# Optimization experiments

Measured on AMD Instinct MI355X. Metric: run time of the kernel, lower is better.

The kernel has to match this reference:

```python
import jax, jax.numpy as jnp
import numpy as np

B, S, V, H = 32, 512, 32, 128
EPS = 1e-5

def _ln(h, w, b):
    m = jnp.mean(h, axis=-1, keepdims=True)
    var = jnp.mean((h - m) ** 2, axis=-1, keepdims=True)
    return (h - m) * jax.lax.rsqrt(var + EPS) * w + b

def setup_inputs() -> dict:
    key = jax.random.key(0)
    ks = jax.random.split(key, 24)
    n = lambda k, shp: jax.random.normal(k, shp, dtype=jnp.float32) * 0.05
    return {
        "x": jax.random.normal(ks[0], (B, S, V), dtype=jnp.float32),
        # flattened GRN (input_dim=V -> H)
        "fw1": n(ks[1], (H, V)), "fb1": jnp.zeros((H,), jnp.float32),
        "fw2": n(ks[2], (H, H)), "fb2": jnp.zeros((H,), jnp.float32),
        "fgw": n(ks[3], (H, H)), "fgb": jnp.zeros((H,), jnp.float32),
        "fsw": n(ks[4], (H, V)), "fsb": jnp.zeros((H,), jnp.float32),
        "flnw": jnp.ones((H,), jnp.float32), "flnb": jnp.zeros((H,), jnp.float32),
        # V per-variable GRNs (input_dim=1 -> H), stacked on leading V axis
        "vw1": n(ks[5], (V, H)), "vb1": jnp.zeros((V, H), jnp.float32),
        "vw2": n(ks[6], (V, H, H)), "vb2": jnp.zeros((V, H), jnp.float32),
        "vgw": n(ks[7], (V, H, H)), "vgb": jnp.zeros((V, H), jnp.float32),
        "vsw": n(ks[8], (V, H)), "vsb": jnp.zeros((V, H), jnp.float32),
        "vlnw": jnp.ones((V, H), jnp.float32), "vlnb": jnp.zeros((V, H), jnp.float32),
    }

def reference(x, fw1, fb1, fw2, fb2, fgw, fgb, fsw, fsb, flnw, flnb,
              vw1, vb1, vw2, vb2, vgw, vgb, vsw, vsb, vlnw, vlnb):
    # ---- flattened GRN -> variable weights ----
    h = jax.nn.elu(jnp.einsum('bsv,hv->bsh', x, fw1) + fb1)
    h = jnp.einsum('bsh,kh->bsk', h, fw2) + fb2
    g = jax.nn.sigmoid(jnp.einsum('bsh,kh->bsk', h, fgw) + fgb)
    skip = jnp.einsum('bsv,hv->bsh', x, fsw) + fsb
    w_out = _ln(g * h + (1.0 - g) * skip, flnw, flnb)        # [B,S,H]
    weights = jax.nn.softmax(w_out[..., :V], axis=-1)        # [B,S,V]
    # ---- per-variable GRNs, batched over V ----
    xe = x[..., None]                                         # [B,S,V,1]
    hv = jax.nn.elu(xe * vw1 + vb1)                           # [B,S,V,H]
    hv = jnp.einsum('bsvh,vkh->bsvk', hv, vw2) + vb2
    gv = jax.nn.sigmoid(jnp.einsum('bsvh,vkh->bsvk', hv, vgw) + vgb)
    skipv = xe * vsw + vsb                                    # [B,S,V,H]
    vout = _ln(gv * hv + (1.0 - gv) * skipv, vlnw, vlnb)      # [B,S,V,H]
    # ---- softmax-weighted combination ----
    selected = jnp.einsum('bsvh,bsv->bsh', vout, weights)     # [B,S,H]
    return selected, weights
```

## Files before the change

### kernel.cpp

```cpp
#include <hip/hip_runtime.h>
#include <hip/hip_bf16.h>

typedef __bf16 bf16_t;
typedef __bf16 bf16x8 __attribute__((ext_vector_type(8)));
typedef float  f32x4  __attribute__((ext_vector_type(4)));

#define DEVFN static __device__ __forceinline__

constexpr int TOK   = 32 * 512;
constexpr int W_OFF = TOK * 128;

constexpr size_t WS_A_VW2 = 0;
constexpr size_t WS_A_WG2 = (size_t)1 << 20;
constexpr size_t WS_BG2   = (size_t)2 << 20;
constexpr size_t WS_A_FW2 = ((size_t)2 << 20) + (64u  << 10);
constexpr size_t WS_A_WG1 = ((size_t)2 << 20) + (128u << 10);
constexpr size_t WS_BG1   = ((size_t)2 << 20) + (192u << 10);
constexpr size_t WS_A_FW1 = ((size_t)2 << 20) + (224u << 10);
constexpr size_t WS_A_FSW = ((size_t)2 << 20) + (256u << 10);
constexpr size_t WS_PART  = (size_t)3 << 20;
constexpr size_t PART_SZ  = (size_t)TOK * 128 * 4;

DEVFN float eluf(float z)  { return z > 0.0f ? z : (__expf(z) - 1.0f); }
DEVFN float sigmf(float z) { return __builtin_amdgcn_rcpf(1.0f + __expf(-z)); }
DEVFN unsigned short f2bfu(float f){ bf16_t h = (bf16_t)f; return __builtin_bit_cast(unsigned short, h); }

DEVFN uint4 pack8(f32x4 a, f32x4 b){
  uint4 r;
  r.x = (unsigned)f2bfu(a[0]) | ((unsigned)f2bfu(a[1]) << 16);
  r.y = (unsigned)f2bfu(a[2]) | ((unsigned)f2bfu(a[3]) << 16);
  r.z = (unsigned)f2bfu(b[0]) | ((unsigned)f2bfu(b[1]) << 16);
  r.w = (unsigned)f2bfu(b[2]) | ((unsigned)f2bfu(b[3]) << 16);
  return r;
}
DEVFN f32x4 mfma16(bf16x8 a, bf16x8 b, f32x4 c){
  return __builtin_amdgcn_mfma_f32_16x16x32_bf16(a, b, c, 0, 0, 0);
}
DEVFN bf16x8 asbf(uint4 u){ return __builtin_bit_cast(bf16x8, u); }

__global__ void k0_prep(const float* __restrict__ fw1, const float* __restrict__ fw2,
                        const float* __restrict__ fgw, const float* __restrict__ fgb,
                        const float* __restrict__ fb2, const float* __restrict__ fsw,
                        const float* __restrict__ vw2, const float* __restrict__ vgw,
                        const float* __restrict__ vgb, const float* __restrict__ vb2,
                        unsigned char* __restrict__ ws)
{
  const int b = blockIdx.x, tid = threadIdx.x;
  if (b < 256){
    const int v  = b >> 3;
    const int k2 = (b & 7) * 16 + (tid >> 4);
    const int h0 = (tid & 15) * 8;
    const float* gw = vgw + ((size_t)v * 128 + k2) * 128;
    const float* w2 = vw2 + (size_t)v * 128 * 128;
    f32x4 a0 = {0,0,0,0}, a1 = {0,0,0,0};
    for (int k = 0; k < 128; ++k){
      float a = gw[k];
      f32x4 u = *(const f32x4*)(w2 + k*128 + h0);
      f32x4 w = *(const f32x4*)(w2 + k*128 + h0 + 4);
      #pragma unroll
      for (int e = 0; e < 4; ++e){ a0[e] = fmaf(a, u[e], a0[e]); a1[e] = fmaf(a, w[e], a1[e]); }
    }
    unsigned blk = (unsigned)(h0 >> 3) ^ (unsigned)(k2 & 7);
    *(uint4*)(ws + WS_A_WG2 + (size_t)v*32768 + (size_t)k2*256 + blk*16) = pack8(a0, a1);
    if ((b & 7) == 0 && tid < 128){
      const float* gr = vgw + ((size_t)v*128 + tid) * 128;
      const float* vb = vb2 + v*128;
      float s = vgb[v*128 + tid];
      for (int k = 0; k < 128; ++k) s = fmaf(gr[k], vb[k], s);
      ((float*)(ws + WS_BG2))[v*128 + tid] = s;
    }
  } else if (b < 288){
    const int v = b - 256;
    const int k = tid >> 1, hh = (tid & 1) * 64;
    const float* src = vw2 + ((size_t)v*128 + k) * 128;
    #pragma unroll
    for (int i = 0; i < 8; ++i){
      int h0 = hh + i*8;
      f32x4 a = *(const f32x4*)(src + h0);
      f32x4 c = *(const f32x4*)(src + h0 + 4);
      unsigned blk = (unsigned)(h0 >> 3) ^ (unsigned)(k & 7);
      *(uint4*)(ws + WS_A_VW2 + (size_t)v*32768 + (size_t)k*256 + blk*16) = pack8(a, c);
    }
  } else if (b < 296){
    const int k2 = (b - 288) * 16 + (tid >> 4);
    const int h0 = (tid & 15) * 8;
    const float* gw = fgw + (size_t)k2 * 128;
    f32x4 a0 = {0,0,0,0}, a1 = {0,0,0,0};
    for (int k = 0; k < 128; ++k){
      float a = gw[k];
      f32x4 u = *(const f32x4*)(fw2 + k*128 + h0);
      f32x4 w = *(const f32x4*)(fw2 + k*128 + h0 + 4);
      #pragma unroll
      for (int e = 0; e < 4; ++e){ a0[e] = fmaf(a, u[e], a0[e]); a1[e] = fmaf(a, w[e], a1[e]); }
    }
    unsigned blk = (unsigned)(h0 >> 3) ^ (unsigned)(k2 & 7);
    *(uint4*)(ws + WS_A_WG1 + (size_t)k2*256 + blk*16) = pack8(a0, a1);
    if (b == 288 && tid < 128){
      const float* gr = fgw + (size_t)tid * 128;
      float s = fgb[tid];
      for (int k = 0; k < 128; ++k) s = fmaf(gr[k], fb2[k], s);
      ((float*)(ws + WS_BG1))[tid] = s;
    }
  } else if (b == 296){
    const int k = tid >> 1, hh = (tid & 1) * 64;
    const float* src = fw2 + (size_t)k * 128;
    #pragma unroll
    for (int i = 0; i < 8; ++i){
      int h0 = hh + i*8;
      f32x4 a = *(const f32x4*)(src + h0);
      f32x4 c = *(const f32x4*)(src + h0 + 4);
      unsigned blk = (unsigned)(h0 >> 3) ^ (unsigned)(k & 7);
      *(uint4*)(ws + WS_A_FW2 + (size_t)k*256 + blk*16) = pack8(a, c);
    }
  } else if (b == 297){
    const int k = tid >> 1, v0 = (tid & 1) * 16;
    #pragma unroll
    for (int i = 0; i < 2; ++i){
      f32x4 a  = *(const f32x4*)(fw1 + k*32 + v0 + i*8);
      f32x4 c  = *(const f32x4*)(fw1 + k*32 + v0 + i*8 + 4);
      *(uint4*)(ws + WS_A_FW1 + (size_t)k*64 + (size_t)v0*2 + i*16) = pack8(a, c);
      f32x4 a2 = *(const f32x4*)(fsw + k*32 + v0 + i*8);
      f32x4 c2 = *(const f32x4*)(fsw + k*32 + v0 + i*8 + 4);
      *(uint4*)(ws + WS_A_FSW + (size_t)k*64 + (size_t)v0*2 + i*16) = pack8(a2, c2);
    }
  }
}

__global__ __launch_bounds__(256) void k1_flat(
  const float* __restrict__ x,   const float* __restrict__ fb1,
  const float* __restrict__ fb2, const float* __restrict__ fsb,
  const float* __restrict__ flnw,const float* __restrict__ flnb,
  const unsigned char* __restrict__ ws, float* __restrict__ out)
{
  __shared__ __align__(16) unsigned char ldsW[65536];
  __shared__ __align__(16) unsigned char ldsH[4][4096];
  const int tid = threadIdx.x;
  const int wid = tid >> 6, lane = tid & 63;
  const int tl = lane & 15, q = lane >> 4;
  const int t0 = blockIdx.x * 64;
  const int tw = t0 + wid * 16 + tl;

  {
    const uint4* s1 = (const uint4*)(ws + WS_A_FW2);
    const uint4* s2 = (const uint4*)(ws + WS_A_WG1);
    uint4* d1 = (uint4*)ldsW;
    uint4* d2 = (uint4*)(ldsW + 32768);
    #pragma unroll
    for (int i = 0; i < 8; ++i){ d1[tid + i*256] = s1[tid + i*256]; d2[tid + i*256] = s2[tid + i*256]; }
  }
  bf16x8 xf;
  {
    f32x4 a = *(const f32x4*)(x + (size_t)tw*32 + q*8);
    f32x4 c = *(const f32x4*)(x + (size_t)tw*32 + q*8 + 4);
    #pragma unroll
    for (int e = 0; e < 4; ++e){ xf[e] = (bf16_t)a[e]; xf[e+4] = (bf16_t)c[e]; }
  }
  __syncthreads();

  const unsigned swzt = (unsigned)(tl & 7) << 4;
  #pragma unroll
  for (int mt = 0; mt < 8; ++mt){
    const int row = mt*16 + tl;
    uint4 araw = *(const uint4*)(ws + WS_A_FW1 + (size_t)row*64 + q*16);
    f32x4 acc = *(const f32x4*)(fb1 + mt*16 + q*4);
    acc = mfma16(asbf(araw), xf, acc);
    ushort4 hb;
    hb.x = f2bfu(eluf(acc[0])); hb.y = f2bfu(eluf(acc[1]));
    hb.z = f2bfu(eluf(acc[2])); hb.w = f2bfu(eluf(acc[3]));
    *(ushort4*)(ldsH[wid] + (unsigned)tl*256 + (((unsigned)(mt*32 + q*8)) ^ swzt)) = hb;
  }
  bf16x8 h1f[4];
  #pragma unroll
  for (int kb = 0; kb < 4; ++kb)
    h1f[kb] = asbf(*(const uint4*)(ldsH[wid] + (unsigned)tl*256 + (((unsigned)(kb*64 + q*16)) ^ swzt)));

  f32x4 wo[8];
  const float* bg1p = (const float*)(ws + WS_BG1);
  #pragma unroll
  for (int mt = 0; mt < 8; ++mt){
    const int row = mt*16 + tl;
    const uint4* aw = (const uint4*)(ldsW + (size_t)row*256);
    const uint4* ag = (const uint4*)(ldsW + 32768 + (size_t)row*256);
    const unsigned rsw = (unsigned)(row & 7);
    f32x4 h2 = *(const f32x4*)(fb2 + mt*16 + q*4);
    f32x4 gp = *(const f32x4*)(bg1p + mt*16 + q*4);
    #pragma unroll
    for (int kb = 0; kb < 4; ++kb){
      unsigned blk = (unsigned)(kb*4 + q) ^ rsw;
      h2 = mfma16(asbf(aw[blk]), h1f[kb], h2);
      gp = mfma16(asbf(ag[blk]), h1f[kb], gp);
    }
    uint4 asr = *(const uint4*)(ws + WS_A_FSW + (size_t)row*64 + q*16);
    f32x4 sk = *(const f32x4*)(fsb + mt*16 + q*4);
    sk = mfma16(asbf(asr), xf, sk);
    #pragma unroll
    for (int r = 0; r < 4; ++r){
      float g = sigmf(gp[r]);
      wo[mt][r] = sk[r] + g * (h2[r] - sk[r]);
    }
  }
  float sm = 0.f, sq = 0.f;
  #pragma unroll
  for (int mt = 0; mt < 8; ++mt)
  #pragma unroll
  for (int r = 0; r < 4; ++r){ float p = wo[mt][r]; sm += p; sq = fmaf(p, p, sq); }
  sm += __shfl_xor(sm, 16); sm += __shfl_xor(sm, 32);
  sq += __shfl_xor(sq, 16); sq += __shfl_xor(sq, 32);
  const float mean = sm * (1.f/128.f);
  const float var  = sq * (1.f/128.f) - mean*mean;
  const float rs   = __builtin_amdgcn_rsqf(var + 1e-5f);
  float wv[8];
  #pragma unroll
  for (int mt = 0; mt < 2; ++mt){
    f32x4 lw = *(const f32x4*)(flnw + mt*16 + q*4);
    f32x4 lb = *(const f32x4*)(flnb + mt*16 + q*4);
    #pragma unroll
    for (int r = 0; r < 4; ++r) wv[mt*4+r] = (wo[mt][r] - mean) * rs * lw[r] + lb[r];
  }
  float mx = wv[0];
  #pragma unroll
  for (int j = 1; j < 8; ++j) mx = fmaxf(mx, wv[j]);
  mx = fmaxf(mx, __shfl_xor(mx, 16)); mx = fmaxf(mx, __shfl_xor(mx, 32));
  float se = 0.f;
  #pragma unroll
  for (int j = 0; j < 8; ++j){ wv[j] = __expf(wv[j] - mx); se += wv[j]; }
  se += __shfl_xor(se, 16); se += __shfl_xor(se, 32);
  const float inv = __builtin_amdgcn_rcpf(se);
  #pragma unroll
  for (int mt = 0; mt < 2; ++mt)
  #pragma unroll
  for (int r = 0; r < 4; ++r)
    out[(size_t)W_OFF + (size_t)tw*32 + mt*16 + q*4 + r] = wv[mt*4+r] * inv;
}

__global__ __launch_bounds__(512, 1) void k2_main(
  const float* __restrict__ x,   const float* __restrict__ vw1,
  const float* __restrict__ vb1, const float* __restrict__ vb2,
  const float* __restrict__ vsw, const float* __restrict__ vsb,
  const float* __restrict__ vlnw,const float* __restrict__ vlnb,
  const unsigned char* __restrict__ ws, float* __restrict__ out,
  float* __restrict__ part, int nvg)
{
  __shared__ __align__(16) uint4 slab[8192];
  const int tid = threadIdx.x;
  const int wid = tid >> 6, lane = tid & 63;
  const int tl = lane & 15, q = lane >> 4;
  const int bid = blockIdx.x;
  const int c   = bid & 63;
  const int g   = bid >> 6;
  const int VPG = 32 / nvg;
  const int vbase = g * VPG;
  const int t0 = ((c & 7) * 8 + (c >> 3)) * 256;
  const int ta = t0 + wid * 32 + tl, tb = ta + 16;
  const float* bg2p = (const float*)(ws + WS_BG2);
  float* __restrict__ dst = (g == nvg - 1) ? out : (part + (size_t)g * TOK * 128);

  auto stage = [&](int buf, int v){
    const uint4* sa = (const uint4*)(ws + WS_A_VW2 + (size_t)v*32768) + tid;
    const uint4* sg = (const uint4*)(ws + WS_A_WG2 + (size_t)v*32768) + tid;
    uint4* da = slab + buf*4096 + tid;
    uint4* dg = slab + buf*4096 + 2048 + tid;
    #pragma unroll
    for (int i = 0; i < 4; ++i)
      __builtin_amdgcn_global_load_lds(
        (const __attribute__((address_space(1))) void*)(sa + i*512),
        (__attribute__((address_space(3))) void*)(da + i*512), 16, 0, 0);
    #pragma unroll
    for (int i = 0; i < 4; ++i)
      __builtin_amdgcn_global_load_lds(
        (const __attribute__((address_space(1))) void*)(sg + i*512),
        (__attribute__((address_space(3))) void*)(dg + i*512), 16, 0, 0);
  };

  stage(0, vbase);
  __syncthreads();

  f32x4 sel[2][8];
  #pragma unroll
  for (int mt = 0; mt < 8; ++mt){ sel[0][mt] = (f32x4){0,0,0,0}; sel[1][mt] = (f32x4){0,0,0,0}; }

  int cur = 0;
  for (int vi = 0; vi < VPG; ++vi){
    const int v = vbase + vi;
    if (vi + 1 < VPG) stage(cur ^ 1, v + 1);

    const float xv0 = x[(size_t)ta*32 + v];
    const float xv1 = x[(size_t)tb*32 + v];
    const float wt0 = out[(size_t)W_OFF + (size_t)ta*32 + v];
    const float wt1 = out[(size_t)W_OFF + (size_t)tb*32 + v];

    bf16x8 bf0[4], bf1[4];
    #pragma unroll
    for (int kb = 0; kb < 4; ++kb){
      const float* wp = vw1 + v*128 + kb*32 + q*8;
      const float* bp = vb1 + v*128 + kb*32 + q*8;
      f32x4 w0v = *(const f32x4*)wp, w1v = *(const f32x4*)(wp + 4);
      f32x4 b0v = *(const f32x4*)bp, b1v = *(const f32x4*)(bp + 4);
      bf16x8 f0, f1;
      #pragma unroll
      for (int e = 0; e < 4; ++e){
        f0[e]   = (bf16_t)eluf(fmaf(xv0, w0v[e], b0v[e]));
        f0[e+4] = (bf16_t)eluf(fmaf(xv0, w1v[e], b1v[e]));
        f1[e]   = (bf16_t)eluf(fmaf(xv1, w0v[e], b0v[e]));
        f1[e+4] = (bf16_t)eluf(fmaf(xv1, w1v[e], b1v[e]));
      }
      bf0[kb] = f0; bf1[kb] = f1;
    }

    const uint4* sl = slab + cur*4096;
    f32x4 pre[8][2];
    #pragma unroll
    for (int mt = 0; mt < 8; ++mt){
      const int row = mt*16 + tl;
      const uint4* arow = sl + row*16;
      const uint4* grow = sl + 2048 + row*16;
      const unsigned rsw = (unsigned)(row & 7);
      f32x4 bini = *(const f32x4*)(vb2 + v*128 + mt*16 + q*4);
      f32x4 gini = *(const f32x4*)(bg2p + v*128 + mt*16 + q*4);
      f32x4 h0 = bini, h1 = bini, g0 = gini, g1 = gini;
      #pragma unroll
      for (int kb = 0; kb < 4; ++kb){
        const unsigned blk = (unsigned)(kb*4 + q) ^ rsw;
        bf16x8 a = asbf(arow[blk]);
        bf16x8 gg = asbf(grow[blk]);
        h0 = mfma16(a, bf0[kb], h0);
        h1 = mfma16(a, bf1[kb], h1);
        g0 = mfma16(gg, bf0[kb], g0);
        g1 = mfma16(gg, bf1[kb], g1);
      }
      f32x4 sw_ = *(const f32x4*)(vsw + v*128 + mt*16 + q*4);
      f32x4 sb_ = *(const f32x4*)(vsb + v*128 + mt*16 + q*4);
      #pragma unroll
      for (int r = 0; r < 4; ++r){
        float sk0 = fmaf(xv0, sw_[r], sb_[r]);
        float sk1 = fmaf(xv1, sw_[r], sb_[r]);
        pre[mt][0][r] = sk0 + sigmf(g0[r]) * (h0[r] - sk0);
        pre[mt][1][r] = sk1 + sigmf(g1[r]) * (h1[r] - sk1);
      }
    }

    #pragma unroll
    for (int nt = 0; nt < 2; ++nt){
      const float wt = nt ? wt1 : wt0;
      float sm = 0.f, sq = 0.f;
      #pragma unroll
      for (int mt = 0; mt < 8; ++mt)
      #pragma unroll
      for (int r = 0; r < 4; ++r){ float p = pre[mt][nt][r]; sm += p; sq = fmaf(p, p, sq); }
      sm += __shfl_xor(sm, 16); sm += __shfl_xor(sm, 32);
      sq += __shfl_xor(sq, 16); sq += __shfl_xor(sq, 32);
      const float mean = sm * (1.f/128.f);
      const float var  = sq * (1.f/128.f) - mean*mean;
      const float rsq  = __builtin_amdgcn_rsqf(var + 1e-5f);
      const float c1   = wt * rsq;
      #pragma unroll
      for (int mt = 0; mt < 8; ++mt){
        f32x4 lw = *(const f32x4*)(vlnw + v*128 + mt*16 + q*4);
        f32x4 lb = *(const f32x4*)(vlnb + v*128 + mt*16 + q*4);
        #pragma unroll
        for (int r = 0; r < 4; ++r)
          sel[nt][mt][r] = fmaf((pre[mt][nt][r] - mean) * lw[r], c1,
                                fmaf(wt, lb[r], sel[nt][mt][r]));
      }
    }

    __syncthreads();
    cur ^= 1;
  }

  #pragma unroll
  for (int mt = 0; mt < 8; ++mt){
    *(f32x4*)(dst + (size_t)ta*128 + mt*16 + q*4) = sel[0][mt];
    *(f32x4*)(dst + (size_t)tb*128 + mt*16 + q*4) = sel[1][mt];
  }
}

__global__ __launch_bounds__(256) void k3_reduce(float* __restrict__ out,
                                                 const float* __restrict__ part,
                                                 int nparts)
{
  const size_t idx = (size_t)blockIdx.x * 256 + threadIdx.x;
  f32x4 s = ((const f32x4*)out)[idx];
  for (int g = 0; g < nparts; ++g){
    f32x4 p = ((const f32x4*)part)[(size_t)g * TOK * 32 + idx];
    #pragma unroll
    for (int r = 0; r < 4; ++r) s[r] += p[r];
  }
  ((f32x4*)out)[idx] = s;
}

extern "C" void kernel_launch(void* const* d_in, const int* in_sizes, int n_in,
                              void* d_out, int out_size, void* d_ws, size_t ws_size,
                              hipStream_t stream)
{
  (void)in_sizes; (void)n_in; (void)out_size;
  const float* x    = (const float*)d_in[0];
  const float* fw1  = (const float*)d_in[1];
  const float* fb1  = (const float*)d_in[2];
  const float* fw2  = (const float*)d_in[3];
  const float* fb2  = (const float*)d_in[4];
  const float* fgw  = (const float*)d_in[5];
  const float* fgb  = (const float*)d_in[6];
  const float* fsw  = (const float*)d_in[7];
  const float* fsb  = (const float*)d_in[8];
  const float* flnw = (const float*)d_in[9];
  const float* flnb = (const float*)d_in[10];
  const float* vw1  = (const float*)d_in[11];
  const float* vb1  = (const float*)d_in[12];
  const float* vw2  = (const float*)d_in[13];
  const float* vb2  = (const float*)d_in[14];
  const float* vgw  = (const float*)d_in[15];
  const float* vgb  = (const float*)d_in[16];
  const float* vsw  = (const float*)d_in[17];
  const float* vsb  = (const float*)d_in[18];
  const float* vlnw = (const float*)d_in[19];
  const float* vlnb = (const float*)d_in[20];
  float* out = (float*)d_out;
  unsigned char* ws = (unsigned char*)d_ws;
  float* part = (float*)(ws + WS_PART);

  k0_prep<<<298, 256, 0, stream>>>(fw1, fw2, fgw, fgb, fb2, fsw, vw2, vgw, vgb, vb2, ws);
  k1_flat<<<256, 256, 0, stream>>>(x, fb1, fb2, fsb, flnw, flnb, ws, out);

  if (ws_size >= WS_PART + 3 * PART_SZ){
    k2_main<<<256, 512, 0, stream>>>(x, vw1, vb1, vb2, vsw, vsb, vlnw, vlnb,
                                     ws, out, part, 4);
    k3_reduce<<<2048, 256, 0, stream>>>(out, part, 3);
  } else if (ws_size >= WS_PART + PART_SZ){
    k2_main<<<128, 512, 0, stream>>>(x, vw1, vb1, vb2, vsw, vsb, vlnw, vlnb,
                                     ws, out, part, 2);
    k3_reduce<<<2048, 256, 0, stream>>>(out, part, 1);
  } else {
    k2_main<<<64, 512, 0, stream>>>(x, vw1, vb1, vb2, vsw, vsb, vlnw, vlnb,
                                    ws, out, part, 1);
  }
}
```

Baseline: 148.1 us.

## Shrink k2 blocks to 256 threads and single-buffer weight slab via register copies

```diff
diff --git a/kernel.cpp b/kernel.cpp
--- a/kernel.cpp
+++ b/kernel.cpp
@@ -233,7 +233,7 @@
     out[(size_t)W_OFF + (size_t)tw*32 + mt*16 + q*4 + r] = wv[mt*4+r] * inv;
 }
 
-__global__ __launch_bounds__(512, 1) void k2_main(
+__global__ __launch_bounds__(256, 1) void k2_main(
   const float* __restrict__ x,   const float* __restrict__ vw1,
   const float* __restrict__ vb1, const float* __restrict__ vb2,
   const float* __restrict__ vsw, const float* __restrict__ vsb,
@@ -241,49 +241,36 @@
   const unsigned char* __restrict__ ws, float* __restrict__ out,
   float* __restrict__ part, int nvg)
 {
-  __shared__ __align__(16) uint4 slab[8192];
+  __shared__ __align__(16) uint4 slab[4096];
   const int tid = threadIdx.x;
   const int wid = tid >> 6, lane = tid & 63;
   const int tl = lane & 15, q = lane >> 4;
   const int bid = blockIdx.x;
-  const int c   = bid & 63;
-  const int g   = bid >> 6;
+  const int c   = bid & 127;
+  const int g   = bid >> 7;
   const int VPG = 32 / nvg;
   const int vbase = g * VPG;
-  const int t0 = ((c & 7) * 8 + (c >> 3)) * 256;
+  const int t0 = ((c & 7) * 16 + (c >> 3)) * 128;
   const int ta = t0 + wid * 32 + tl, tb = ta + 16;
   const float* bg2p = (const float*)(ws + WS_BG2);
   float* __restrict__ dst = (g == nvg - 1) ? out : (part + (size_t)g * TOK * 128);
 
-  auto stage = [&](int buf, int v){
-    const uint4* sa = (const uint4*)(ws + WS_A_VW2 + (size_t)v*32768) + tid;
-    const uint4* sg = (const uint4*)(ws + WS_A_WG2 + (size_t)v*32768) + tid;
-    uint4* da = slab + buf*4096 + tid;
-    uint4* dg = slab + buf*4096 + 2048 + tid;
-    #pragma unroll
-    for (int i = 0; i < 4; ++i)
-      __builtin_amdgcn_global_load_lds(
-        (const __attribute__((address_space(1))) void*)(sa + i*512),
-        (__attribute__((address_space(3))) void*)(da + i*512), 16, 0, 0);
-    #pragma unroll
-    for (int i = 0; i < 4; ++i)
-      __builtin_amdgcn_global_load_lds(
-        (const __attribute__((address_space(1))) void*)(sg + i*512),
-        (__attribute__((address_space(3))) void*)(dg + i*512), 16, 0, 0);
-  };
-
-  stage(0, vbase);
+  {
+    const uint4* sa = (const uint4*)(ws + WS_A_VW2 + (size_t)vbase*32768);
+    const uint4* sg = (const uint4*)(ws + WS_A_WG2 + (size_t)vbase*32768);
+    #pragma unroll
+    for (int i = 0; i < 8; ++i) slab[tid + i*256] = sa[tid + i*256];
+    #pragma unroll
+    for (int i = 0; i < 8; ++i) slab[2048 + tid + i*256] = sg[tid + i*256];
+  }
   __syncthreads();
 
   f32x4 sel[2][8];
   #pragma unroll
   for (int mt = 0; mt < 8; ++mt){ sel[0][mt] = (f32x4){0,0,0,0}; sel[1][mt] = (f32x4){0,0,0,0}; }
 
-  int cur = 0;
   for (int vi = 0; vi < VPG; ++vi){
     const int v = vbase + vi;
-    if (vi + 1 < VPG) stage(cur ^ 1, v + 1);
-
     const float xv0 = x[(size_t)ta*32 + v];
     const float xv1 = x[(size_t)tb*32 + v];
     const float wt0 = out[(size_t)W_OFF + (size_t)ta*32 + v];
@@ -307,13 +294,12 @@
       bf0[kb] = f0; bf1[kb] = f1;
     }
 
-    const uint4* sl = slab + cur*4096;
     f32x4 pre[8][2];
     #pragma unroll
     for (int mt = 0; mt < 8; ++mt){
       const int row = mt*16 + tl;
-      const uint4* arow = sl + row*16;
-      const uint4* grow = sl + 2048 + row*16;
+      const uint4* arow = slab + row*16;
+      const uint4* grow = slab + 2048 + row*16;
       const unsigned rsw = (unsigned)(row & 7);
       f32x4 bini = *(const f32x4*)(vb2 + v*128 + mt*16 + q*4);
       f32x4 gini = *(const f32x4*)(bg2p + v*128 + mt*16 + q*4);
@@ -321,10 +307,10 @@
       #pragma unroll
       for (int kb = 0; kb < 4; ++kb){
         const unsigned blk = (unsigned)(kb*4 + q) ^ rsw;
-        bf16x8 a = asbf(arow[blk]);
+        bf16x8 a  = asbf(arow[blk]);
         bf16x8 gg = asbf(grow[blk]);
-        h0 = mfma16(a, bf0[kb], h0);
-        h1 = mfma16(a, bf1[kb], h1);
+        h0 = mfma16(a,  bf0[kb], h0);
+        h1 = mfma16(a,  bf1[kb], h1);
         g0 = mfma16(gg, bf0[kb], g0);
         g1 = mfma16(gg, bf1[kb], g1);
       }
@@ -365,7 +351,15 @@
     }
 
     __syncthreads();
-    cur ^= 1;
+    if (vi + 1 < VPG){
+      const uint4* sa = (const uint4*)(ws + WS_A_VW2 + (size_t)(v+1)*32768);
+      const uint4* sg = (const uint4*)(ws + WS_A_WG2 + (size_t)(v+1)*32768);
+      #pragma unroll
+      for (int i = 0; i < 8; ++i) slab[tid + i*256] = sa[tid + i*256];
+      #pragma unroll
+      for (int i = 0; i < 8; ++i) slab[2048 + tid + i*256] = sg[tid + i*256];
+      __syncthreads();
+    }
   }
 
   #pragma unroll
@@ -423,15 +417,15 @@
   k1_flat<<<256, 256, 0, stream>>>(x, fb1, fb2, fsb, flnw, flnb, ws, out);
 
   if (ws_size >= WS_PART + 3 * PART_SZ){
-    k2_main<<<256, 512, 0, stream>>>(x, vw1, vb1, vb2, vsw, vsb, vlnw, vlnb,
+    k2_main<<<512, 256, 0, stream>>>(x, vw1, vb1, vb2, vsw, vsb, vlnw, vlnb,
                                      ws, out, part, 4);
     k3_reduce<<<2048, 256, 0, stream>>>(out, part, 3);
   } else if (ws_size >= WS_PART + PART_SZ){
-    k2_main<<<128, 512, 0, stream>>>(x, vw1, vb1, vb2, vsw, vsb, vlnw, vlnb,
+    k2_main<<<256, 256, 0, stream>>>(x, vw1, vb1, vb2, vsw, vsb, vlnw, vlnb,
                                      ws, out, part, 2);
     k3_reduce<<<2048, 256, 0, stream>>>(out, part, 1);
   } else {
-    k2_main<<<64, 512, 0, stream>>>(x, vw1, vb1, vb2, vsw, vsb, vlnw, vlnb,
-                                    ws, out, part, 1);
-  }
-}
+    k2_main<<<128, 256, 0, stream>>>(x, vw1, vb1, vb2, vsw, vsb, vlnw, vlnb,
+                                     ws, out, part, 1);
+  }
+}
```

New measurement: 177.1 us. +19.6%, slower.
